# Optimization experiments

Measured on AMD Instinct MI355X. Metric: run time of the kernel, lower is better.

The kernel has to match this reference:

```python
import jax, jax.numpy as jnp
import numpy as np

B, S, HID = 2, 1024, 2048
H, D, KV = 32, 64, 8          # query heads, head dim, kv heads (GQA)
INNER = H * D                 # 2048
KV_DIM = KV * D               # 512


def setup_inputs() -> dict:
    key = jax.random.key(0)
    ks = jax.random.split(key, 12)
    s = 0.02
    return {
        "query": jax.random.normal(ks[0], (B, S, HID), jnp.float32),
        "key": jax.random.normal(ks[1], (B, S, HID), jnp.float32),
        "value": jax.random.normal(ks[2], (B, S, HID), jnp.float32),
        "mask": jnp.zeros((B, 1, S, S), jnp.float32),
        "position_bias": jax.random.normal(ks[3], (1, H, S, S), jnp.float32),
        "Wq": jax.random.normal(ks[4], (HID, INNER), jnp.float32) * s,
        "bq": jnp.zeros((INNER,), jnp.float32),
        "Wk": jax.random.normal(ks[5], (HID, KV_DIM), jnp.float32) * s,
        "bk": jnp.zeros((KV_DIM,), jnp.float32),
        "Wv": jax.random.normal(ks[6], (HID, KV_DIM), jnp.float32) * s,
        "bv": jnp.zeros((KV_DIM,), jnp.float32),
        "Wo": jax.random.normal(ks[7], (INNER, HID), jnp.float32) * s,
        "bo": jnp.zeros((HID,), jnp.float32),
    }


def reference(query, key, value, mask, position_bias, Wq, bq, Wk, bk, Wv, bv, Wo, bo):
    # projections (torch nn.Linear equivalent, weights stored [in,out])
    q = (query @ Wq + bq).reshape(B, S, H, D)     # [B,S,H,D]
    k = (key @ Wk + bk).reshape(B, S, KV, D)      # [B,S,KV,D]
    v = (value @ Wv + bv).reshape(B, S, KV, D)
    rep = H // KV
    k = jnp.repeat(k, rep, axis=2)                # GQA repeat_kv -> [B,S,H,D]
    v = jnp.repeat(v, rep, axis=2)
    scores = jnp.einsum("bqhd,bkhd->bhqk", q, k)  # [B,H,S,S]
    scores = (scores + position_bias) * (1.0 / jnp.sqrt(jnp.float32(D)))
    scores = scores + mask
    probs = jax.nn.softmax(scores.astype(jnp.float32), axis=-1).astype(q.dtype)
    out = jnp.einsum("bhqk,bkhd->bqhd", probs, v).reshape(B, S, INNER)
    return out @ Wo + bo                          # [B,S,HID]
```

## Files before the change

### kernel.cpp

```cpp
#include <hip/hip_runtime.h>
#include <stdint.h>

#define DEVI __device__ __forceinline__

typedef __attribute__((ext_vector_type(8))) short bf16x8;
typedef __attribute__((ext_vector_type(4))) float f32x4;
typedef __attribute__((ext_vector_type(4))) float flt4;
typedef __attribute__((ext_vector_type(8))) unsigned short u16x8;
typedef __attribute__((ext_vector_type(4))) unsigned short u16x4;

DEVI unsigned short f2bf(float f){
  union{float f;uint32_t u;}v; v.f=f;
  uint32_t u=v.u;
  u += 0x7FFFu + ((u>>16)&1u);
  return (unsigned short)(u>>16);
}

DEVI uint32_t cvt_pk_bf16(float lo, float hi){
  uint32_t r;
  asm("v_cvt_pk_bf16_f32 %0, %1, %2" : "=v"(r) : "v"(lo), "v"(hi));
  return r;
}

DEVI float fexp2(float x){
#if __has_builtin(__builtin_amdgcn_exp2f)
  return __builtin_amdgcn_exp2f(x);
#else
  return exp2f(x);
#endif
}

DEVI void gload16(const void* g, void* l){
  __builtin_amdgcn_global_load_lds((const __attribute__((address_space(1))) void*)g,
                                   (__attribute__((address_space(3))) void*)l, 16, 0, 0);
}

__global__ void cvt3_k(const float* __restrict__ q, const float* __restrict__ k,
                       const float* __restrict__ v, unsigned short* __restrict__ qb,
                       unsigned short* __restrict__ kb, unsigned short* __restrict__ vb, int n8){
  int i = blockIdx.x*256 + threadIdx.x;
  if (i >= n8) return;
  const float* src = blockIdx.y==0 ? q : (blockIdx.y==1 ? k : v);
  unsigned short* dst = blockIdx.y==0 ? qb : (blockIdx.y==1 ? kb : vb);
  const flt4* s = (const flt4*)src;
  flt4 a = s[2*i], b = s[2*i+1];
  u16x8 o;
  o[0]=f2bf(a.x); o[1]=f2bf(a.y); o[2]=f2bf(a.z); o[3]=f2bf(a.w);
  o[4]=f2bf(b.x); o[5]=f2bf(b.y); o[6]=f2bf(b.z); o[7]=f2bf(b.w);
  ((u16x8*)dst)[i] = o;
}

__global__ void wtrans_all(const float* __restrict__ Wq, const float* __restrict__ Wk,
                           const float* __restrict__ Wv, const float* __restrict__ Wo,
                           unsigned short* __restrict__ WqT, unsigned short* __restrict__ WkT,
                           unsigned short* __restrict__ WvT, unsigned short* __restrict__ WoT){
  __shared__ float tile[64][65];
  const int K = 2048;
  int id = blockIdx.x;
  const float* W; unsigned short* WT; int N, tt;
  if (id < 1024)      { W=Wq; WT=WqT; N=2048; tt=id; }
  else if (id < 1280) { W=Wk; WT=WkT; N=512;  tt=id-1024; }
  else if (id < 1536) { W=Wv; WT=WvT; N=512;  tt=id-1280; }
  else                { W=Wo; WT=WoT; N=2048; tt=id-1536; }
  int sh = (N==2048) ? 5 : 3;
  int n0 = (tt & ((1<<sh)-1))*64, k0 = (tt >> sh)*64;
  int t = threadIdx.x;
  int r = t>>4, c4 = (t&15)*4;
  #pragma unroll
  for (int i=0;i<4;i++){
    flt4 v = *(const flt4*)&W[(size_t)(k0 + r + i*16)*N + n0 + c4];
    tile[r+i*16][c4+0]=v.x; tile[r+i*16][c4+1]=v.y; tile[r+i*16][c4+2]=v.z; tile[r+i*16][c4+3]=v.w;
  }
  __syncthreads();
  #pragma unroll
  for (int i=0;i<4;i++){
    int rn = r + i*16;
    u16x4 o;
    o[0]=f2bf(tile[c4+0][rn]); o[1]=f2bf(tile[c4+1][rn]);
    o[2]=f2bf(tile[c4+2][rn]); o[3]=f2bf(tile[c4+3][rn]);
    *(u16x4*)&WT[(size_t)(n0+rn)*K + k0 + c4] = o;
  }
}

#define GEMM64_KSTEP(A_, BT_, K_)                                              \
    __syncthreads();                                                           \
    _Pragma("unroll")                                                          \
    for (int j=0;j<2;j++){                                                     \
      int cid = (j*4+w)*64 + l;                                                \
      int row = cid>>3, sl = cid&7;                                            \
      int gsl = sl ^ (row&7);                                                  \
      gload16(&A_ [(size_t)(m0+row)*K_ + k0 + gsl*8], &As[(j*4+w)*512]);       \
      gload16(&BT_[(size_t)(n0+row)*K_ + k0 + gsl*8], &Bs[(j*4+w)*512]);       \
    }                                                                          \
    __syncthreads();                                                           \
    _Pragma("unroll")                                                          \
    for (int kk=0;kk<2;kk++){                                                  \
      bf16x8 af[2], bfv[2];                                                    \
      _Pragma("unroll")                                                        \
      for (int mt=0;mt<2;mt++){                                                \
        int row = wr+mt*16+lq;                                                 \
        af[mt] = *(const bf16x8*)&As[row*64 + (((kk*4+lg)^(lq&7))*8)];         \
      }                                                                        \
      _Pragma("unroll")                                                        \
      for (int nt=0;nt<2;nt++){                                                \
        int row = wc+nt*16+lq;                                                 \
        bfv[nt] = *(const bf16x8*)&Bs[row*64 + (((kk*4+lg)^(lq&7))*8)];        \
      }                                                                        \
      _Pragma("unroll")                                                        \
      for (int mt=0;mt<2;mt++)                                                 \
        _Pragma("unroll")                                                      \
        for (int nt=0;nt<2;nt++)                                               \
          acc[mt][nt] = __builtin_amdgcn_mfma_f32_16x16x32_bf16(af[mt], bfv[nt], acc[mt][nt], 0,0,0); \
    }

__global__ __launch_bounds__(256) void qkv64(const unsigned short* __restrict__ qbf,
    const unsigned short* __restrict__ kbf, const unsigned short* __restrict__ vbf,
    const unsigned short* __restrict__ WqT, const unsigned short* __restrict__ WkT,
    const unsigned short* __restrict__ WvT,
    const float* __restrict__ bq, const float* __restrict__ bk, const float* __restrict__ bv,
    unsigned short* __restrict__ Qp, unsigned short* __restrict__ Kp, unsigned short* __restrict__ VTb){
  __shared__ unsigned short As[64*64];
  __shared__ unsigned short Bs[64*64];
  const int K = 2048;
  int id = blockIdx.x;
  const unsigned short *A, *BT; const float* bias; int N, op, tt;
  if (id < 1024)      { op=0; A=qbf; BT=WqT; bias=bq; N=2048; tt=id; }
  else if (id < 1280) { op=1; A=kbf; BT=WkT; bias=bk; N=512;  tt=id-1024; }
  else                { op=2; A=vbf; BT=WvT; bias=bv; N=512;  tt=id-1280; }
  int sh = (N==2048) ? 5 : 3;
  int n0 = (tt & ((1<<sh)-1))*64, m0 = (tt >> sh)*64;
  int t = threadIdx.x, w = t>>6, l = t&63;
  int lq = l&15, lg = l>>4;
  int wr = (w>>1)*32, wc = (w&1)*32;
  f32x4 acc[2][2] = {};
  for (int k0=0;k0<K;k0+=64){
    GEMM64_KSTEP(A, BT, K)
  }
  #pragma unroll
  for (int nt=0;nt<2;nt++){
    int col = n0 + wc + nt*16 + lq;
    float bvl = bias[col];
    #pragma unroll
    for (int mt=0;mt<2;mt++){
      #pragma unroll
      for (int r=0;r<4;r++){
        int row = m0 + wr + mt*16 + lg*4 + r;
        float v = acc[mt][nt][r] + bvl;
        if (op==0)      Qp[(size_t)row*2048 + col] = f2bf(v);
        else if (op==1) Kp[(size_t)row*512 + col] = f2bf(v);
        else {
          int b = row>>10, s = row&1023;
          VTb[((size_t)(b*512 + col)<<10) + s] = f2bf(v);
        }
      }
    }
  }
}

__global__ __launch_bounds__(256) void oproj64(const unsigned short* __restrict__ A,
    const unsigned short* __restrict__ BT, const float* __restrict__ bias,
    float* __restrict__ Cout){
  __shared__ unsigned short As[64*64];
  __shared__ unsigned short Bs[64*64];
  const int K = 2048, N = 2048;
  int n0 = blockIdx.x*64, m0 = blockIdx.y*64;
  int t = threadIdx.x, w = t>>6, l = t&63;
  int lq = l&15, lg = l>>4;
  int wr = (w>>1)*32, wc = (w&1)*32;
  f32x4 acc[2][2] = {};
  for (int k0=0;k0<K;k0+=64){
    GEMM64_KSTEP(A, BT, K)
  }
  #pragma unroll
  for (int nt=0;nt<2;nt++){
    int col = n0 + wc + nt*16 + lq;
    float bvl = bias[col];
    #pragma unroll
    for (int mt=0;mt<2;mt++){
      #pragma unroll
      for (int r=0;r<4;r++){
        int row = m0 + wr + mt*16 + lg*4 + r;
        Cout[(size_t)row*N + col] = acc[mt][nt][r] + bvl;
      }
    }
  }
}

__global__ __launch_bounds__(256,4) void attn_k(const unsigned short* __restrict__ Q,
    const unsigned short* __restrict__ Kp, const unsigned short* __restrict__ VT,
    const float* __restrict__ pbias, const float* __restrict__ mask,
    unsigned short* __restrict__ Oout){
  __shared__ unsigned short Ks[2][4096];
  __shared__ unsigned short VTs[2][4096];
  __shared__ unsigned short Pb[4][1024];
  int t=threadIdx.x, w=t>>6, l=t&63;
  int qt=blockIdx.x, h=blockIdx.y, b=blockIdx.z;
  int kv=h>>2;
  int lq = l&15, lg = l>>4;
  int q0 = qt*64 + w*16;
  bf16x8 qf0, qf1;
  {
    const unsigned short* qp = &Q[((size_t)(b*1024 + q0 + lq))*2048 + h*64 + lg*8];
    qf0 = *(const bf16x8*)qp;
    qf1 = *(const bf16x8*)(qp + 32);
  }
  const float* pbase = &pbias[((size_t)h*1024 + (q0+lq))*1024];
  const float* mbase = &mask [((size_t)b*1024 + (q0+lq))*1024];
  f32x4 oacc[4] = {};
  float psum = 0.f;
  const float L2E  = 1.4426950408889634f;
  const float SCL2E = 0.125f*1.4426950408889634f;
  const float FIXM = 16.0f;
  unsigned short* pw = &Pb[w][0];
  int swz = (lq&7)<<3;

  flt4 praw[4], mraw[4];
  flt4 comb[4];

#define ATTN_STAGE(buf_, kt_)                                                          \
  _Pragma("unroll")                                                                    \
  for (int j=0;j<2;j++){                                                               \
    int cid = (j*4+w)*64 + l;                                                          \
    int row = cid>>3, sl = cid&7;                                                      \
    int gsl = sl ^ (row&7);                                                            \
    gload16(&Kp[((size_t)(b*1024 + (kt_)*64 + row))*512 + kv*64 + gsl*8], &Ks[buf_][(j*4+w)*512]);          \
    gload16(&VT[((size_t)(b*512 + kv*64 + row))*1024 + (size_t)((kt_)*64 + gsl*8)], &VTs[buf_][(j*4+w)*512]);\
  }

#define ATTN_LOADRAW(kt_)                                                              \
  _Pragma("unroll")                                                                    \
  for (int nt=0;nt<4;nt++){                                                            \
    praw[nt] = *(const flt4*)&pbase[(kt_)*64 + nt*16 + lg*4];                          \
    mraw[nt] = *(const flt4*)&mbase[(kt_)*64 + nt*16 + lg*4];                          \
  }

#define ATTN_COMBINE()                                                                 \
  _Pragma("unroll")                                                                    \
  for (int nt=0;nt<4;nt++)                                                             \
    _Pragma("unroll")                                                                  \
    for (int r=0;r<4;r++)                                                              \
      comb[nt][r] = (praw[nt][r]*0.125f + mraw[nt][r] - FIXM)*L2E;

  ATTN_STAGE(0, 0)
  ATTN_LOADRAW(0)
  __syncthreads();
  ATTN_COMBINE()

  for (int kt=0;kt<16;kt++){
    int cur = kt&1;
    if (kt < 15){
      ATTN_STAGE(cur^1, kt+1)
      ATTN_LOADRAW(kt+1)
    }
    f32x4 sacc[4] = {};
    __builtin_amdgcn_s_setprio(1);
    #pragma unroll
    for (int nt=0;nt<4;nt++){
      int row = nt*16 + lq;
      bf16x8 kf0 = *(const bf16x8*)&Ks[cur][row*64 + (( lg    ^ (row&7))*8)];
      bf16x8 kf1 = *(const bf16x8*)&Ks[cur][row*64 + (((4+lg) ^ (row&7))*8)];
      sacc[nt] = __builtin_amdgcn_mfma_f32_16x16x32_bf16(kf0, qf0, sacc[nt], 0,0,0);
      sacc[nt] = __builtin_amdgcn_mfma_f32_16x16x32_bf16(kf1, qf1, sacc[nt], 0,0,0);
    }
    __builtin_amdgcn_s_setprio(0);
    #pragma unroll
    for (int nt=0;nt<4;nt++){
      float p0 = fexp2(fmaf(sacc[nt][0], SCL2E, comb[nt][0]));
      float p1 = fexp2(fmaf(sacc[nt][1], SCL2E, comb[nt][1]));
      float p2 = fexp2(fmaf(sacc[nt][2], SCL2E, comb[nt][2]));
      float p3 = fexp2(fmaf(sacc[nt][3], SCL2E, comb[nt][3]));
      psum += (p0+p1)+(p2+p3);
      uint2 pk;
      pk.x = cvt_pk_bf16(p0,p1);
      pk.y = cvt_pk_bf16(p2,p3);
      *(uint2*)&pw[lq*64 + ((nt*16 + lg*4) ^ swz)] = pk;
    }
    #pragma unroll
    for (int kk=0;kk<2;kk++){
      bf16x8 pa = *(const bf16x8*)&pw[lq*64 + ((kk*32 + lg*8) ^ swz)];
      __builtin_amdgcn_s_setprio(1);
      #pragma unroll
      for (int nt=0;nt<4;nt++){
        int vrow = nt*16 + lq;
        bf16x8 vf = *(const bf16x8*)&VTs[cur][vrow*64 + (((kk*4+lg) ^ (vrow&7))*8)];
        oacc[nt] = __builtin_amdgcn_mfma_f32_16x16x32_bf16(pa, vf, oacc[nt], 0,0,0);
      }
      __builtin_amdgcn_s_setprio(0);
    }
    if (kt < 15){
      __syncthreads();
      ATTN_COMBINE()
    }
  }
  float lsum = psum;
  lsum += __shfl_xor(lsum, 16);
  lsum += __shfl_xor(lsum, 32);
  #pragma unroll
  for (int r=0;r<4;r++){
    float lr = __shfl(lsum, lg*4 + r);
    float linv = 1.f/lr;
    int qrow = q0 + lg*4 + r;
    #pragma unroll
    for (int nt=0;nt<4;nt++){
      Oout[((size_t)(b*1024 + qrow))*2048 + h*64 + nt*16 + lq] = f2bf(oacc[nt][r]*linv);
    }
  }
#undef ATTN_STAGE
#undef ATTN_LOADRAW
#undef ATTN_COMBINE
}

extern "C" void kernel_launch(void* const* d_in, const int* in_sizes, int n_in,
                              void* d_out, int out_size, void* d_ws, size_t ws_size,
                              hipStream_t stream){
  (void)in_sizes; (void)n_in; (void)out_size; (void)ws_size;
  const float* query = (const float*)d_in[0];
  const float* key   = (const float*)d_in[1];
  const float* value = (const float*)d_in[2];
  const float* mask  = (const float*)d_in[3];
  const float* pbias = (const float*)d_in[4];
  const float* Wq = (const float*)d_in[5];
  const float* bq = (const float*)d_in[6];
  const float* Wk = (const float*)d_in[7];
  const float* bk = (const float*)d_in[8];
  const float* Wv = (const float*)d_in[9];
  const float* bv = (const float*)d_in[10];
  const float* Wo = (const float*)d_in[11];
  const float* bo = (const float*)d_in[12];
  char* ws = (char*)d_ws;
  const size_t MB = (size_t)1<<20;
  unsigned short* qbf = (unsigned short*)(ws + 0*MB);
  unsigned short* kbf = (unsigned short*)(ws + 8*MB);
  unsigned short* vbf = (unsigned short*)(ws + 16*MB);
  unsigned short* WqT = (unsigned short*)(ws + 24*MB);
  unsigned short* WkT = (unsigned short*)(ws + 32*MB);
  unsigned short* WvT = (unsigned short*)(ws + 34*MB);
  unsigned short* WoT = (unsigned short*)(ws + 36*MB);
  unsigned short* Qp  = (unsigned short*)(ws + 44*MB);
  unsigned short* Kp  = (unsigned short*)(ws + 52*MB);
  unsigned short* VTb = (unsigned short*)(ws + 54*MB);
  unsigned short* Aout= (unsigned short*)(ws + 56*MB);

  cvt3_k<<<dim3(2048,3),256,0,stream>>>(query, key, value, qbf, kbf, vbf, 524288);
  wtrans_all<<<2560,256,0,stream>>>(Wq, Wk, Wv, Wo, WqT, WkT, WvT, WoT);
  qkv64<<<1536,256,0,stream>>>(qbf, kbf, vbf, WqT, WkT, WvT, bq, bk, bv, Qp, Kp, VTb);
  attn_k<<<dim3(16,32,2),256,0,stream>>>(Qp, Kp, VTb, pbias, mask, Aout);
  oproj64<<<dim3(32,32),256,0,stream>>>(Aout, WoT, bo, (float*)d_out);
}
```

Baseline: 179.4 us.

## Prefetch position bias and mask two tiles ahead with explicit vmcnt waits

```diff
diff --git a/kernel.cpp b/kernel.cpp
--- a/kernel.cpp
+++ b/kernel.cpp
@@ -186,7 +186,7 @@
   }
 }
 
-__global__ __launch_bounds__(256,4) void attn_k(const unsigned short* __restrict__ Q,
+__global__ __launch_bounds__(256,3) void attn_k(const unsigned short* __restrict__ Q,
     const unsigned short* __restrict__ Kp, const unsigned short* __restrict__ VT,
     const float* __restrict__ pbias, const float* __restrict__ mask,
     unsigned short* __restrict__ Oout){
@@ -208,14 +208,15 @@
   const float* mbase = &mask [((size_t)b*1024 + (q0+lq))*1024];
   f32x4 oacc[4] = {};
   float psum = 0.f;
-  const float L2E  = 1.4426950408889634f;
+  const float L2E   = 1.4426950408889634f;
   const float SCL2E = 0.125f*1.4426950408889634f;
-  const float FIXM = 16.0f;
+  const float NFM   = -16.0f*1.4426950408889634f;
   unsigned short* pw = &Pb[w][0];
   int swz = (lq&7)<<3;
 
-  flt4 praw[4], mraw[4];
-  flt4 comb[4];
+  flt4 rpA[4], rmA[4], rpB[4], rmB[4], comb[4];
+
+#define SB __builtin_amdgcn_sched_barrier(0)
 
 #define ATTN_STAGE(buf_, kt_)                                                          \
   _Pragma("unroll")                                                                    \
@@ -227,71 +228,93 @@
     gload16(&VT[((size_t)(b*512 + kv*64 + row))*1024 + (size_t)((kt_)*64 + gsl*8)], &VTs[buf_][(j*4+w)*512]);\
   }
 
-#define ATTN_LOADRAW(kt_)                                                              \
+#define ATTN_RAW(RP_, RM_, kt_)                                                        \
   _Pragma("unroll")                                                                    \
   for (int nt=0;nt<4;nt++){                                                            \
-    praw[nt] = *(const flt4*)&pbase[(kt_)*64 + nt*16 + lg*4];                          \
-    mraw[nt] = *(const flt4*)&mbase[(kt_)*64 + nt*16 + lg*4];                          \
-  }
-
-#define ATTN_COMBINE()                                                                 \
+    RP_[nt] = *(const flt4*)&pbase[(kt_)*64 + nt*16 + lg*4];                           \
+    RM_[nt] = *(const flt4*)&mbase[(kt_)*64 + nt*16 + lg*4];                           \
+  }
+
+#define ATTN_COMBINE(RP_, RM_)                                                         \
   _Pragma("unroll")                                                                    \
   for (int nt=0;nt<4;nt++)                                                             \
     _Pragma("unroll")                                                                  \
     for (int r=0;r<4;r++)                                                              \
-      comb[nt][r] = (praw[nt][r]*0.125f + mraw[nt][r] - FIXM)*L2E;
-
-  ATTN_STAGE(0, 0)
-  ATTN_LOADRAW(0)
-  __syncthreads();
-  ATTN_COMBINE()
-
-  for (int kt=0;kt<16;kt++){
-    int cur = kt&1;
-    if (kt < 15){
-      ATTN_STAGE(cur^1, kt+1)
-      ATTN_LOADRAW(kt+1)
-    }
-    f32x4 sacc[4] = {};
-    __builtin_amdgcn_s_setprio(1);
-    #pragma unroll
-    for (int nt=0;nt<4;nt++){
-      int row = nt*16 + lq;
-      bf16x8 kf0 = *(const bf16x8*)&Ks[cur][row*64 + (( lg    ^ (row&7))*8)];
-      bf16x8 kf1 = *(const bf16x8*)&Ks[cur][row*64 + (((4+lg) ^ (row&7))*8)];
-      sacc[nt] = __builtin_amdgcn_mfma_f32_16x16x32_bf16(kf0, qf0, sacc[nt], 0,0,0);
-      sacc[nt] = __builtin_amdgcn_mfma_f32_16x16x32_bf16(kf1, qf1, sacc[nt], 0,0,0);
-    }
-    __builtin_amdgcn_s_setprio(0);
-    #pragma unroll
-    for (int nt=0;nt<4;nt++){
-      float p0 = fexp2(fmaf(sacc[nt][0], SCL2E, comb[nt][0]));
-      float p1 = fexp2(fmaf(sacc[nt][1], SCL2E, comb[nt][1]));
-      float p2 = fexp2(fmaf(sacc[nt][2], SCL2E, comb[nt][2]));
-      float p3 = fexp2(fmaf(sacc[nt][3], SCL2E, comb[nt][3]));
-      psum += (p0+p1)+(p2+p3);
-      uint2 pk;
-      pk.x = cvt_pk_bf16(p0,p1);
-      pk.y = cvt_pk_bf16(p2,p3);
-      *(uint2*)&pw[lq*64 + ((nt*16 + lg*4) ^ swz)] = pk;
-    }
-    #pragma unroll
-    for (int kk=0;kk<2;kk++){
-      bf16x8 pa = *(const bf16x8*)&pw[lq*64 + ((kk*32 + lg*8) ^ swz)];
-      __builtin_amdgcn_s_setprio(1);
-      #pragma unroll
-      for (int nt=0;nt<4;nt++){
-        int vrow = nt*16 + lq;
-        bf16x8 vf = *(const bf16x8*)&VTs[cur][vrow*64 + (((kk*4+lg) ^ (vrow&7))*8)];
-        oacc[nt] = __builtin_amdgcn_mfma_f32_16x16x32_bf16(pa, vf, oacc[nt], 0,0,0);
-      }
-      __builtin_amdgcn_s_setprio(0);
-    }
-    if (kt < 15){
-      __syncthreads();
-      ATTN_COMBINE()
-    }
-  }
+      comb[nt][r] = fmaf(RP_[nt][r], SCL2E, fmaf(RM_[nt][r], L2E, NFM));
+
+#define ATTN_COMPUTE(P_)                                                               \
+  {                                                                                    \
+    f32x4 sacc[4] = {};                                                                \
+    __builtin_amdgcn_s_setprio(1);                                                     \
+    _Pragma("unroll")                                                                  \
+    for (int nt=0;nt<4;nt++){                                                          \
+      int row = nt*16 + lq;                                                            \
+      bf16x8 kf0 = *(const bf16x8*)&Ks[P_][row*64 + (( lg    ^ (row&7))*8)];           \
+      bf16x8 kf1 = *(const bf16x8*)&Ks[P_][row*64 + (((4+lg) ^ (row&7))*8)];           \
+      sacc[nt] = __builtin_amdgcn_mfma_f32_16x16x32_bf16(kf0, qf0, sacc[nt], 0,0,0);   \
+      sacc[nt] = __builtin_amdgcn_mfma_f32_16x16x32_bf16(kf1, qf1, sacc[nt], 0,0,0);   \
+    }                                                                                  \
+    __builtin_amdgcn_s_setprio(0);                                                     \
+    _Pragma("unroll")                                                                  \
+    for (int nt=0;nt<4;nt++){                                                          \
+      float p0 = fexp2(fmaf(sacc[nt][0], SCL2E, comb[nt][0]));                         \
+      float p1 = fexp2(fmaf(sacc[nt][1], SCL2E, comb[nt][1]));                         \
+      float p2 = fexp2(fmaf(sacc[nt][2], SCL2E, comb[nt][2]));                         \
+      float p3 = fexp2(fmaf(sacc[nt][3], SCL2E, comb[nt][3]));                         \
+      psum += (p0+p1)+(p2+p3);                                                         \
+      uint2 pk;                                                                        \
+      pk.x = cvt_pk_bf16(p0,p1);                                                       \
+      pk.y = cvt_pk_bf16(p2,p3);                                                       \
+      *(uint2*)&pw[lq*64 + ((nt*16 + lg*4) ^ swz)] = pk;                               \
+    }                                                                                  \
+    _Pragma("unroll")                                                                  \
+    for (int kk=0;kk<2;kk++){                                                          \
+      bf16x8 pa = *(const bf16x8*)&pw[lq*64 + ((kk*32 + lg*8) ^ swz)];                 \
+      __builtin_amdgcn_s_setprio(1);                                                   \
+      _Pragma("unroll")                                                                \
+      for (int nt=0;nt<4;nt++){                                                        \
+        int vrow = nt*16 + lq;                                                         \
+        bf16x8 vf = *(const bf16x8*)&VTs[P_][vrow*64 + (((kk*4+lg) ^ (vrow&7))*8)];    \
+        oacc[nt] = __builtin_amdgcn_mfma_f32_16x16x32_bf16(pa, vf, oacc[nt], 0,0,0);   \
+      }                                                                                \
+      __builtin_amdgcn_s_setprio(0);                                                   \
+    }                                                                                  \
+  }
+
+#define HALF_ITER(kt_, P_, RP_, RM_)                                                   \
+  {                                                                                    \
+    ATTN_COMBINE(RP_, RM_); SB;                                                        \
+    ATTN_STAGE((P_)^1, (kt_)+1); SB;                                                   \
+    ATTN_RAW(RP_, RM_, (kt_)+2); SB;                                                   \
+    asm volatile("s_waitcnt vmcnt(20)" ::: "memory");                                  \
+    __builtin_amdgcn_s_barrier(); SB;                                                  \
+    ATTN_COMPUTE(P_); SB;                                                              \
+    __builtin_amdgcn_s_barrier();                                                      \
+  }
+
+  ATTN_RAW(rpA, rmA, 0); SB;
+  ATTN_STAGE(0, 0); SB;
+  ATTN_RAW(rpB, rmB, 1); SB;
+
+  for (int kb=0; kb<14; kb+=2){
+    HALF_ITER(kb+0, 0, rpA, rmA)
+    HALF_ITER(kb+1, 1, rpB, rmB)
+  }
+  {
+    ATTN_COMBINE(rpA, rmA); SB;
+    ATTN_STAGE(1, 15); SB;
+    asm volatile("s_waitcnt vmcnt(12)" ::: "memory");
+    __builtin_amdgcn_s_barrier(); SB;
+    ATTN_COMPUTE(0); SB;
+    __builtin_amdgcn_s_barrier();
+  }
+  {
+    ATTN_COMBINE(rpB, rmB); SB;
+    asm volatile("s_waitcnt vmcnt(0)" ::: "memory");
+    __builtin_amdgcn_s_barrier(); SB;
+    ATTN_COMPUTE(1);
+  }
+
   float lsum = psum;
   lsum += __shfl_xor(lsum, 16);
   lsum += __shfl_xor(lsum, 32);
@@ -305,9 +328,12 @@
       Oout[((size_t)(b*1024 + qrow))*2048 + h*64 + nt*16 + lq] = f2bf(oacc[nt][r]*linv);
     }
   }
+#undef HALF_ITER
+#undef ATTN_COMPUTE
+#undef ATTN_COMBINE
+#undef ATTN_RAW
 #undef ATTN_STAGE
-#undef ATTN_LOADRAW
-#undef ATTN_COMBINE
+#undef SB
 }
 
 extern "C" void kernel_launch(void* const* d_in, const int* in_sizes, int n_in,
```

Result: slower. 197.3 us (+10.0%).
